# Kernel tuning notes

Hardware: AMD Instinct MI355X
Metric: run time of the kernel (lower is better)

The kernel has to match this reference:

```python
import math
import jax, jax.numpy as jnp
import numpy as np

D = 1024
H = 16
DK = D // H
B = 4
L = 2048


def setup_inputs() -> dict:
    key = jax.random.key(0)
    ks = jax.random.split(key, 11)
    s = 1.0 / math.sqrt(D)
    return {
        "q": jax.random.normal(ks[0], (B, L, D), jnp.float32),
        "k": jax.random.normal(ks[1], (B, L, D), jnp.float32),
        "v": jax.random.normal(ks[2], (B, L, D), jnp.float32),
        "wq_w": jax.random.normal(ks[3], (D, D), jnp.float32) * s,
        "wq_b": jnp.zeros((D,), jnp.float32),
        "wk_w": jax.random.normal(ks[4], (D, D), jnp.float32) * s,
        "wk_b": jnp.zeros((D,), jnp.float32),
        "wv_w": jax.random.normal(ks[5], (D, D), jnp.float32) * s,
        "wv_b": jnp.zeros((D,), jnp.float32),
        "wo_w": jax.random.normal(ks[6], (D, D), jnp.float32) * s,
        "wo_b": jnp.zeros((D,), jnp.float32),
    }


def reference(q, k, v, wq_w, wq_b, wk_w, wk_b, wv_w, wv_b, wo_w, wo_b):
    # torch Linear: x @ W.T + b
    Q = (q @ wq_w.T + wq_b).reshape(B, L, H, DK).transpose(0, 2, 1, 3)  # [B,H,L,DK]
    K = (k @ wk_w.T + wk_b).reshape(B, -1, H, DK).transpose(0, 2, 1, 3)
    V = (v @ wv_w.T + wv_b).reshape(B, -1, H, DK).transpose(0, 2, 1, 3)
    sc = jnp.einsum("bhqd,bhkd->bhqk", Q, K) / math.sqrt(DK)  # [B,H,L,L]
    # causal mask: strictly upper triangular filled with -1e9
    cm = jnp.triu(jnp.ones((L, L), dtype=bool), 1)
    sc = jnp.where(cm, jnp.float32(-1e9), sc)
    at = jax.nn.softmax(sc, axis=-1)  # dropout p=0 (eval)
    out = jnp.einsum("bhqk,bhkd->bhqd", at, V)  # [B,H,L,DK]
    out = out.transpose(0, 2, 1, 3).reshape(B, L, D)
    return out @ wo_w.T + wo_b
```

## Files before the change

kernel.cpp:

```cpp
#include <hip/hip_runtime.h>
#include <stdint.h>

#define DD 1024
#define NH 16
#define DHEAD 64
#define NB 4
#define SEQ 2048
#define MR (NB*SEQ)
#define NT (SEQ/128)

typedef __attribute__((ext_vector_type(8))) short s8v;
typedef __attribute__((ext_vector_type(4))) float f4v;

__device__ __forceinline__ unsigned short f2bf(float f) {
  union { float f; uint32_t u; } c; c.f = f;
  uint32_t u = c.u;
  u += 0x7fffu + ((u >> 16) & 1u);
  return (unsigned short)(u >> 16);
}
__device__ __forceinline__ unsigned short f2bf_trunc(float f) {
  union { float f; uint32_t u; } c; c.f = f;
  return (unsigned short)(c.u >> 16);
}

__device__ __forceinline__ void load_lds16(const void* g, void* lds) {
  __builtin_amdgcn_global_load_lds(
      (__attribute__((address_space(1))) void*)(uintptr_t)g,
      (__attribute__((address_space(3))) void*)(uint32_t)(uintptr_t)lds,
      16, 0, 0);
}

__device__ __forceinline__ s8v pack8(float4 a, float4 b) {
  union { unsigned short us[8]; s8v v; } t;
  t.us[0] = f2bf(a.x); t.us[1] = f2bf(a.y); t.us[2] = f2bf(a.z); t.us[3] = f2bf(a.w);
  t.us[4] = f2bf(b.x); t.us[5] = f2bf(b.y); t.us[6] = f2bf(b.z); t.us[7] = f2bf(b.w);
  return t.v;
}

__global__ void cvt_w(
    const float* __restrict__ w0, const float* __restrict__ w1,
    const float* __restrict__ w2, const float* __restrict__ w3,
    unsigned short* __restrict__ d0, unsigned short* __restrict__ d1,
    unsigned short* __restrict__ d2, unsigned short* __restrict__ d3)
{
  int blk = blockIdx.x;
  int a = blk >> 9;
  const float* src = a == 0 ? w0 : (a == 1 ? w1 : (a == 2 ? w2 : w3));
  unsigned short* dst = a == 0 ? d0 : (a == 1 ? d1 : (a == 2 ? d2 : d3));
  size_t i = (size_t)(blk & 511) * 2048 + (size_t)threadIdx.x * 8;
  float4 a4 = *(const float4*)(src + i);
  float4 b4 = *(const float4*)(src + i + 4);
  union { unsigned short us[8]; uint4 u; } t;
  t.us[0] = f2bf(a4.x); t.us[1] = f2bf(a4.y); t.us[2] = f2bf(a4.z); t.us[3] = f2bf(a4.w);
  t.us[4] = f2bf(b4.x); t.us[5] = f2bf(b4.y); t.us[6] = f2bf(b4.z); t.us[7] = f2bf(b4.w);
  *(uint4*)(dst + i) = t.u;
}

__global__ __launch_bounds__(256, 2) void gemm_bt(
    const unsigned short* __restrict__ A,
    const unsigned short* __restrict__ Bw,
    const float* __restrict__ bias,
    float* __restrict__ Cout)
{
  __shared__ __align__(16) short As[64 * 64];
  __shared__ __align__(16) short Bs[128 * 64];
  const int linear = blockIdx.y * 8 + blockIdx.x;
  const int nx = linear >> 7;
  const int my = linear & 127;
  const int tid = threadIdx.x;
  const int wave = tid >> 6, lane = tid & 63;
  const int wm = (wave >> 1) * 32, wn = (wave & 1) * 64;
  const int lr = lane & 15, lg = lane >> 4;
  const int sw = lr & 7;
  const unsigned short* Ab = A + (size_t)my * 64 * DD;
  const unsigned short* Bb = Bw + (size_t)nx * 128 * DD;

  f4v z = {0.f, 0.f, 0.f, 0.f};
  f4v acc[2][4];
  for (int mi = 0; mi < 2; mi++) for (int ni = 0; ni < 4; ni++) acc[mi][ni] = z;

  for (int k0 = 0; k0 < DD; k0 += 64) {
    __syncthreads();
    for (int i = 0; i < 2; i++) {
      int c = tid + i * 256;
      int row = c >> 3, pg = c & 7;
      load_lds16(Ab + (size_t)row * DD + k0 + ((pg ^ (row & 7)) << 3), As + c * 8);
    }
    for (int i = 0; i < 4; i++) {
      int c = tid + i * 256;
      int row = c >> 3, pg = c & 7;
      load_lds16(Bb + (size_t)row * DD + k0 + ((pg ^ (row & 7)) << 3), Bs + c * 8);
    }
    __syncthreads();
    for (int kk = 0; kk < 64; kk += 32) {
      int gb = kk >> 3;
      s8v af[2], bf[4];
      for (int i = 0; i < 2; i++)
        af[i] = *(const s8v*)(As + (wm + i * 16 + lr) * 64 + (((gb + lg) ^ sw) << 3));
      for (int i = 0; i < 4; i++)
        bf[i] = *(const s8v*)(Bs + (wn + i * 16 + lr) * 64 + (((gb + lg) ^ sw) << 3));
      for (int mi = 0; mi < 2; mi++)
        for (int ni = 0; ni < 4; ni++)
          acc[mi][ni] = __builtin_amdgcn_mfma_f32_16x16x32_bf16(af[mi], bf[ni], acc[mi][ni], 0, 0, 0);
    }
  }
  for (int ni = 0; ni < 4; ni++) {
    int col = nx * 128 + wn + ni * 16 + lr;
    float bv = bias[col];
    for (int mi = 0; mi < 2; mi++) {
      int row0 = my * 64 + wm + mi * 16 + lg * 4;
      for (int r = 0; r < 4; r++)
        Cout[(size_t)(row0 + r) * DD + col] = acc[mi][ni][r] + bv;
    }
  }
}

__global__ __launch_bounds__(256, 2) void gemm_qkv(
    const float* __restrict__ qA, const float* __restrict__ kA,
    const float* __restrict__ vA,
    const unsigned short* __restrict__ wq, const unsigned short* __restrict__ wk,
    const unsigned short* __restrict__ wv,
    const float* __restrict__ bq, const float* __restrict__ bk, const float* __restrict__ bv,
    unsigned short* __restrict__ Qp, unsigned short* __restrict__ Kp,
    unsigned short* __restrict__ VpT)
{
  __shared__ __align__(16) short As[128 * 64];
  __shared__ __align__(16) short Bs[128 * 64];
  const int linear = blockIdx.y * 24 + blockIdx.x;
  const int nx  = linear / 192;
  const int rem = linear % 192;
  const int seg = rem >> 6;
  const int my  = rem & 63;
  const float* A          = seg == 0 ? qA : (seg == 1 ? kA : vA);
  const unsigned short* Bw = seg == 0 ? wq : (seg == 1 ? wk : wv);
  const float* bias        = seg == 0 ? bq : (seg == 1 ? bk : bv);

  const int tid = threadIdx.x;
  const int wave = tid >> 6, lane = tid & 63;
  const int wm = (wave >> 1) * 64, wn = (wave & 1) * 64;
  const int lr = lane & 15, lg = lane >> 4;
  const int sw = lr & 7;
  const float* Ab = A + (size_t)my * 128 * DD;
  const unsigned short* Bb = Bw + (size_t)nx * 128 * DD;

  int arow[4], ag[4];
  s8v areg[4];
  for (int i = 0; i < 4; i++) {
    int c = tid + i * 256;
    arow[i] = c >> 3; ag[i] = c & 7;
  }
  for (int i = 0; i < 4; i++) {
    const float* src = Ab + (size_t)arow[i] * DD + (ag[i] << 3);
    areg[i] = pack8(*(const float4*)src, *(const float4*)(src + 4));
  }

  f4v z = {0.f, 0.f, 0.f, 0.f};
  f4v acc[4][4];
  for (int mi = 0; mi < 4; mi++) for (int ni = 0; ni < 4; ni++) acc[mi][ni] = z;

  for (int k0 = 0; k0 < DD; k0 += 64) {
    __syncthreads();
    for (int i = 0; i < 4; i++)
      *(s8v*)(As + arow[i] * 64 + ((ag[i] ^ (arow[i] & 7)) << 3)) = areg[i];
    for (int i = 0; i < 4; i++) {
      int c = tid + i * 256;
      int row = c >> 3, pg = c & 7;
      load_lds16(Bb + (size_t)row * DD + k0 + ((pg ^ (row & 7)) << 3), Bs + c * 8);
    }
    __syncthreads();
    if (k0 + 64 < DD) {
      for (int i = 0; i < 4; i++) {
        const float* src = Ab + (size_t)arow[i] * DD + k0 + 64 + (ag[i] << 3);
        areg[i] = pack8(*(const float4*)src, *(const float4*)(src + 4));
      }
    }
    for (int kk = 0; kk < 64; kk += 32) {
      int gb = kk >> 3;
      s8v af[4], bf[4];
      for (int i = 0; i < 4; i++)
        af[i] = *(const s8v*)(As + (wm + i * 16 + lr) * 64 + (((gb + lg) ^ sw) << 3));
      for (int i = 0; i < 4; i++)
        bf[i] = *(const s8v*)(Bs + (wn + i * 16 + lr) * 64 + (((gb + lg) ^ sw) << 3));
      for (int mi = 0; mi < 4; mi++)
        for (int ni = 0; ni < 4; ni++)
          acc[mi][ni] = __builtin_amdgcn_mfma_f32_16x16x32_bf16(af[mi], bf[ni], acc[mi][ni], 0, 0, 0);
    }
  }
  if (seg < 2) {
    unsigned short* Cout = seg == 0 ? Qp : Kp;
    for (int ni = 0; ni < 4; ni++) {
      int col = nx * 128 + wn + ni * 16 + lr;
      float bv = bias[col];
      for (int mi = 0; mi < 4; mi++) {
        int row0 = my * 128 + wm + mi * 16 + lg * 4;
        for (int r = 0; r < 4; r++)
          Cout[(size_t)(row0 + r) * DD + col] = f2bf(acc[mi][ni][r] + bv);
      }
    }
  } else {
    for (int ni = 0; ni < 4; ni++) {
      int col = nx * 128 + wn + ni * 16 + lr;
      float bv = bias[col];
      int hh = col >> 6, dd = col & 63;
      for (int mi = 0; mi < 4; mi++) {
        int row0 = my * 128 + wm + mi * 16 + lg * 4;
        int bb = row0 >> 11, ll = row0 & 2047;
        uint64_t w = 0;
        for (int r = 0; r < 4; r++)
          w |= (uint64_t)f2bf(acc[mi][ni][r] + bv) << (16 * r);
        *(uint64_t*)(VpT + ((size_t)(bb * NH + hh) * 64 + dd) * SEQ + ll) = w;
      }
    }
  }
}

#define KS_STRIDE 72
#define VT_STRIDE 136
#define PS_STRIDE 72

__device__ __forceinline__ void attn_step(
    const s8v (&qf)[2][2], const s8v (&kf)[2][4],
    f4v (&o)[2][4], float (&ls)[2][4],
    int qbase, int colbase,
    const short* __restrict__ Vt, int vsub, short* __restrict__ Pw,
    int lr, int lg)
{
  const float csc = 0.125f * 1.44269504089f;
  const float FM = 14.0f;
  f4v zv = {0.f, 0.f, 0.f, 0.f};
  f4v s[2][4];
  for (int mi = 0; mi < 2; mi++) for (int ni = 0; ni < 4; ni++) s[mi][ni] = zv;
  for (int ks = 0; ks < 2; ks++)
    for (int mi = 0; mi < 2; mi++)
      for (int ni = 0; ni < 4; ni++)
        s[mi][ni] = __builtin_amdgcn_mfma_f32_16x16x32_bf16(qf[mi][ks], kf[ks][ni], s[mi][ni], 0, 0, 0);
  const bool diag = (colbase + 63 > qbase);
  for (int mi = 0; mi < 2; mi++)
    for (int ni = 0; ni < 4; ni++)
      for (int r = 0; r < 4; r++) {
        float e = __builtin_amdgcn_exp2f(fmaf(s[mi][ni][r], csc, -FM));
        if (diag) {
          int row = qbase + mi * 16 + lg * 4 + r;
          int col = colbase + ni * 16 + lr;
          e = (col > row) ? 0.f : e;
        }
        ls[mi][r] += e;
        Pw[(mi * 16 + lg * 4 + r) * PS_STRIDE + ni * 16 + lr] = (short)f2bf_trunc(e);
      }
  for (int kc2 = 0; kc2 < 2; kc2++) {
    s8v pf[2], vf[4];
    for (int mi = 0; mi < 2; mi++)
      pf[mi] = *(const s8v*)(Pw + (mi * 16 + lr) * PS_STRIDE + kc2 * 32 + lg * 8);
    for (int ni = 0; ni < 4; ni++)
      vf[ni] = *(const s8v*)(Vt + (ni * 16 + lr) * VT_STRIDE + vsub + kc2 * 32 + lg * 8);
    for (int mi = 0; mi < 2; mi++)
      for (int ni = 0; ni < 4; ni++)
        o[mi][ni] = __builtin_amdgcn_mfma_f32_16x16x32_bf16(pf[mi], vf[ni], o[mi][ni], 0, 0, 0);
  }
}

__global__ __launch_bounds__(256, 2) void fattn(
    const unsigned short* __restrict__ Qp,
    const unsigned short* __restrict__ Kp,
    const unsigned short* __restrict__ VpT,
    unsigned short* __restrict__ Op)
{
  __shared__ __align__(16) short Ks[128 * KS_STRIDE];
  __shared__ __align__(16) short Vt[64 * VT_STRIDE];
  __shared__ __align__(16) short Ps[4 * 32 * PS_STRIDE];
  const int tid = threadIdx.x;
  const int wave = tid >> 6, lane = tid & 63;
  const int lr = lane & 15, lg = lane >> 4;
  const int linear = blockIdx.y * 8 + blockIdx.x;
  const int xA = linear >> 6;
  const int bh = linear & 63;
  const int b = bh >> 4, h = bh & 15;
  const int xB = NT - 1 - xA;
  const int qbA = xA * 128 + wave * 32;
  const int qbB = xB * 128 + wave * 32;
  const unsigned short* Qrow = Qp + ((size_t)b * SEQ) * DD + h * DHEAD;
  const unsigned short* Krow = Kp + ((size_t)b * SEQ) * DD + h * DHEAD;
  const unsigned short* VT   = VpT + (size_t)bh * 64 * SEQ;
  short* Pw = Ps + wave * (32 * PS_STRIDE);

  s8v qfA[2][2], qfB[2][2];
  for (int mi = 0; mi < 2; mi++)
    for (int ks = 0; ks < 2; ks++) {
      qfA[mi][ks] = *(const s8v*)(Qrow + (size_t)(qbA + mi * 16 + lr) * DD + ks * 32 + lg * 8);
      qfB[mi][ks] = *(const s8v*)(Qrow + (size_t)(qbB + mi * 16 + lr) * DD + ks * 32 + lg * 8);
    }

  f4v zv = {0.f, 0.f, 0.f, 0.f};
  f4v oA[2][4], oB[2][4];
  float lA[2][4], lB[2][4];
  for (int mi = 0; mi < 2; mi++)
    for (int r = 0; r < 4; r++) { lA[mi][r] = 0.f; lB[mi][r] = 0.f; }
  for (int mi = 0; mi < 2; mi++)
    for (int ni = 0; ni < 4; ni++) { oA[mi][ni] = zv; oB[mi][ni] = zv; }

  const int npair = xB + 1;

  for (int p = 0; p < npair; p++) {
    s8v kreg[4], vreg[4];
    int krow[4], kkc[4], vd[4], vkc[4];
    for (int i = 0; i < 4; i++) {
      int c = tid + i * 256;
      krow[i] = c >> 3; kkc[i] = (c & 7) << 3;
      kreg[i] = *(const s8v*)(Krow + (size_t)(p * 128 + krow[i]) * DD + kkc[i]);
      vd[i] = c >> 4; vkc[i] = (c & 15) << 3;
      vreg[i] = *(const s8v*)(VT + (size_t)vd[i] * SEQ + p * 128 + vkc[i]);
    }
    __syncthreads();
    for (int i = 0; i < 4; i++) {
      *(s8v*)(Ks + krow[i] * KS_STRIDE + kkc[i]) = kreg[i];
      *(s8v*)(Vt + vd[i] * VT_STRIDE + vkc[i]) = vreg[i];
    }
    __syncthreads();
    for (int sub = 0; sub < 2; sub++) {
      int colbase = (2 * p + sub) * 64;
      bool actB = colbase <= qbB + 31;
      bool actA = colbase <= qbA + 31;
      if (actB || actA) {
        const short* KsSub = Ks + sub * 64 * KS_STRIDE;
        s8v kf[2][4];
        for (int ks = 0; ks < 2; ks++)
          for (int ni = 0; ni < 4; ni++)
            kf[ks][ni] = *(const s8v*)(KsSub + (ni * 16 + lr) * KS_STRIDE + ks * 32 + lg * 8);
        int vsub = sub * 64;
        if (actB) attn_step(qfB, kf, oB, lB, qbB, colbase, Vt, vsub, Pw, lr, lg);
        if (actA) attn_step(qfA, kf, oA, lA, qbA, colbase, Vt, vsub, Pw, lr, lg);
      }
    }
  }

  unsigned short* Orow = Op + ((size_t)b * SEQ) * DD + h * DHEAD;
  for (int mi = 0; mi < 2; mi++)
    for (int r = 0; r < 4; r++) {
      float sA = lA[mi][r], sB = lB[mi][r];
      for (int d2 = 1; d2 < 16; d2 <<= 1) {
        sA += __shfl_xor(sA, d2);
        sB += __shfl_xor(sB, d2);
      }
      float invA = 1.f / sA, invB = 1.f / sB;
      size_t rowA = (size_t)qbA + mi * 16 + lg * 4 + r;
      size_t rowB = (size_t)qbB + mi * 16 + lg * 4 + r;
      for (int ni = 0; ni < 4; ni++) {
        Orow[rowA * DD + ni * 16 + lr] = f2bf(oA[mi][ni][r] * invA);
        Orow[rowB * DD + ni * 16 + lr] = f2bf(oB[mi][ni][r] * invB);
      }
    }
}

extern "C" void kernel_launch(void* const* d_in, const int* in_sizes, int n_in,
                              void* d_out, int out_size, void* d_ws, size_t ws_size,
                              hipStream_t stream) {
  const float* q    = (const float*)d_in[0];
  const float* k    = (const float*)d_in[1];
  const float* v    = (const float*)d_in[2];
  const float* wq_w = (const float*)d_in[3];
  const float* wq_b = (const float*)d_in[4];
  const float* wk_w = (const float*)d_in[5];
  const float* wk_b = (const float*)d_in[6];
  const float* wv_w = (const float*)d_in[7];
  const float* wv_b = (const float*)d_in[8];
  const float* wo_w = (const float*)d_in[9];
  const float* wo_b = (const float*)d_in[10];

  const size_t BIG = (size_t)MR * DD;
  const size_t WSZ = (size_t)DD * DD;
  unsigned short* p = (unsigned short*)d_ws;
  unsigned short* wqb = p; p += WSZ;
  unsigned short* wkb = p; p += WSZ;
  unsigned short* wvb = p; p += WSZ;
  unsigned short* wob = p; p += WSZ;
  unsigned short* Qp  = p; p += BIG;
  unsigned short* Kp  = p; p += BIG;
  unsigned short* VpT = p; p += BIG;
  unsigned short* AO  = p; p += BIG;

  cvt_w<<<dim3(2048), dim3(256), 0, stream>>>(
      wq_w, wk_w, wv_w, wo_w, wqb, wkb, wvb, wob);

  gemm_qkv<<<dim3(24, MR / 128), dim3(256), 0, stream>>>(
      q, k, v, wqb, wkb, wvb, wq_b, wk_b, wv_b, Qp, Kp, VpT);

  fattn<<<dim3(NT / 2, NB * NH), dim3(256), 0, stream>>>(Qp, Kp, VpT, AO);

  gemm_bt<<<dim3(8, 128), dim3(256), 0, stream>>>(AO, wob, wo_b, (float*)d_out);

  (void)in_sizes; (void)n_in; (void)out_size; (void)ws_size;
}
```

Measured before the change: 313.1 us.

## Pre-convert QKV activations to bf16 and enlarge output GEMM tile

Adds a separate kernel that converts the q, k and v activations to bf16 in scratch buffers, reusing the AO workspace and the output buffer as scratch. The QKV GEMM can then stage A through direct global-to-LDS loads instead of register loads with in-loop packing. The output projection GEMM moves from 64x128 to 128x128 tiles to get more reuse per block. The cost is an extra full pass that reads and writes the activations, and half as many blocks for the output GEMM.

```diff
diff --git a/kernel.cpp b/kernel.cpp
--- a/kernel.cpp
+++ b/kernel.cpp
@@ -28,13 +28,6 @@
       (__attribute__((address_space(1))) void*)(uintptr_t)g,
       (__attribute__((address_space(3))) void*)(uint32_t)(uintptr_t)lds,
       16, 0, 0);
-}
-
-__device__ __forceinline__ s8v pack8(float4 a, float4 b) {
-  union { unsigned short us[8]; s8v v; } t;
-  t.us[0] = f2bf(a.x); t.us[1] = f2bf(a.y); t.us[2] = f2bf(a.z); t.us[3] = f2bf(a.w);
-  t.us[4] = f2bf(b.x); t.us[5] = f2bf(b.y); t.us[6] = f2bf(b.z); t.us[7] = f2bf(b.w);
-  return t.v;
 }
 
 __global__ void cvt_w(
@@ -56,32 +49,51 @@
   *(uint4*)(dst + i) = t.u;
 }
 
+__global__ void cvt_a(
+    const float* __restrict__ s0, const float* __restrict__ s1,
+    const float* __restrict__ s2,
+    unsigned short* __restrict__ d0, unsigned short* __restrict__ d1,
+    unsigned short* __restrict__ d2)
+{
+  int blk = blockIdx.x;
+  int a = blk >> 12;
+  const float* src = a == 0 ? s0 : (a == 1 ? s1 : s2);
+  unsigned short* dst = a == 0 ? d0 : (a == 1 ? d1 : d2);
+  size_t i = (size_t)(blk & 4095) * 2048 + (size_t)threadIdx.x * 8;
+  float4 a4 = *(const float4*)(src + i);
+  float4 b4 = *(const float4*)(src + i + 4);
+  union { unsigned short us[8]; uint4 u; } t;
+  t.us[0] = f2bf(a4.x); t.us[1] = f2bf(a4.y); t.us[2] = f2bf(a4.z); t.us[3] = f2bf(a4.w);
+  t.us[4] = f2bf(b4.x); t.us[5] = f2bf(b4.y); t.us[6] = f2bf(b4.z); t.us[7] = f2bf(b4.w);
+  *(uint4*)(dst + i) = t.u;
+}
+
 __global__ __launch_bounds__(256, 2) void gemm_bt(
     const unsigned short* __restrict__ A,
     const unsigned short* __restrict__ Bw,
     const float* __restrict__ bias,
     float* __restrict__ Cout)
 {
-  __shared__ __align__(16) short As[64 * 64];
+  __shared__ __align__(16) short As[128 * 64];
   __shared__ __align__(16) short Bs[128 * 64];
   const int linear = blockIdx.y * 8 + blockIdx.x;
-  const int nx = linear >> 7;
-  const int my = linear & 127;
+  const int nx = linear >> 6;
+  const int my = linear & 63;
   const int tid = threadIdx.x;
   const int wave = tid >> 6, lane = tid & 63;
-  const int wm = (wave >> 1) * 32, wn = (wave & 1) * 64;
+  const int wm = (wave >> 1) * 64, wn = (wave & 1) * 64;
   const int lr = lane & 15, lg = lane >> 4;
   const int sw = lr & 7;
-  const unsigned short* Ab = A + (size_t)my * 64 * DD;
+  const unsigned short* Ab = A + (size_t)my * 128 * DD;
   const unsigned short* Bb = Bw + (size_t)nx * 128 * DD;
 
   f4v z = {0.f, 0.f, 0.f, 0.f};
-  f4v acc[2][4];
-  for (int mi = 0; mi < 2; mi++) for (int ni = 0; ni < 4; ni++) acc[mi][ni] = z;
+  f4v acc[4][4];
+  for (int mi = 0; mi < 4; mi++) for (int ni = 0; ni < 4; ni++) acc[mi][ni] = z;
 
   for (int k0 = 0; k0 < DD; k0 += 64) {
     __syncthreads();
-    for (int i = 0; i < 2; i++) {
+    for (int i = 0; i < 4; i++) {
       int c = tid + i * 256;
       int row = c >> 3, pg = c & 7;
       load_lds16(Ab + (size_t)row * DD + k0 + ((pg ^ (row & 7)) << 3), As + c * 8);
@@ -94,12 +106,12 @@
     __syncthreads();
     for (int kk = 0; kk < 64; kk += 32) {
       int gb = kk >> 3;
-      s8v af[2], bf[4];
-      for (int i = 0; i < 2; i++)
+      s8v af[4], bf[4];
+      for (int i = 0; i < 4; i++)
         af[i] = *(const s8v*)(As + (wm + i * 16 + lr) * 64 + (((gb + lg) ^ sw) << 3));
       for (int i = 0; i < 4; i++)
         bf[i] = *(const s8v*)(Bs + (wn + i * 16 + lr) * 64 + (((gb + lg) ^ sw) << 3));
-      for (int mi = 0; mi < 2; mi++)
+      for (int mi = 0; mi < 4; mi++)
         for (int ni = 0; ni < 4; ni++)
           acc[mi][ni] = __builtin_amdgcn_mfma_f32_16x16x32_bf16(af[mi], bf[ni], acc[mi][ni], 0, 0, 0);
     }
@@ -107,8 +119,8 @@
   for (int ni = 0; ni < 4; ni++) {
     int col = nx * 128 + wn + ni * 16 + lr;
     float bv = bias[col];
-    for (int mi = 0; mi < 2; mi++) {
-      int row0 = my * 64 + wm + mi * 16 + lg * 4;
+    for (int mi = 0; mi < 4; mi++) {
+      int row0 = my * 128 + wm + mi * 16 + lg * 4;
       for (int r = 0; r < 4; r++)
         Cout[(size_t)(row0 + r) * DD + col] = acc[mi][ni][r] + bv;
     }
@@ -116,8 +128,8 @@
 }
 
 __global__ __launch_bounds__(256, 2) void gemm_qkv(
-    const float* __restrict__ qA, const float* __restrict__ kA,
-    const float* __restrict__ vA,
+    const unsigned short* __restrict__ qA, const unsigned short* __restrict__ kA,
+    const unsigned short* __restrict__ vA,
     const unsigned short* __restrict__ wq, const unsigned short* __restrict__ wk,
     const unsigned short* __restrict__ wv,
     const float* __restrict__ bq, const float* __restrict__ bk, const float* __restrict__ bv,
@@ -131,7 +143,7 @@
   const int rem = linear % 192;
   const int seg = rem >> 6;
   const int my  = rem & 63;
-  const float* A          = seg == 0 ? qA : (seg == 1 ? kA : vA);
+  const unsigned short* A  = seg == 0 ? qA : (seg == 1 ? kA : vA);
   const unsigned short* Bw = seg == 0 ? wq : (seg == 1 ? wk : wv);
   const float* bias        = seg == 0 ? bq : (seg == 1 ? bk : bv);
 
@@ -140,19 +152,8 @@
   const int wm = (wave >> 1) * 64, wn = (wave & 1) * 64;
   const int lr = lane & 15, lg = lane >> 4;
   const int sw = lr & 7;
-  const float* Ab = A + (size_t)my * 128 * DD;
+  const unsigned short* Ab = A + (size_t)my * 128 * DD;
   const unsigned short* Bb = Bw + (size_t)nx * 128 * DD;
-
-  int arow[4], ag[4];
-  s8v areg[4];
-  for (int i = 0; i < 4; i++) {
-    int c = tid + i * 256;
-    arow[i] = c >> 3; ag[i] = c & 7;
-  }
-  for (int i = 0; i < 4; i++) {
-    const float* src = Ab + (size_t)arow[i] * DD + (ag[i] << 3);
-    areg[i] = pack8(*(const float4*)src, *(const float4*)(src + 4));
-  }
 
   f4v z = {0.f, 0.f, 0.f, 0.f};
   f4v acc[4][4];
@@ -160,20 +161,17 @@
 
   for (int k0 = 0; k0 < DD; k0 += 64) {
     __syncthreads();
-    for (int i = 0; i < 4; i++)
-      *(s8v*)(As + arow[i] * 64 + ((ag[i] ^ (arow[i] & 7)) << 3)) = areg[i];
+    for (int i = 0; i < 4; i++) {
+      int c = tid + i * 256;
+      int row = c >> 3, pg = c & 7;
+      load_lds16(Ab + (size_t)row * DD + k0 + ((pg ^ (row & 7)) << 3), As + c * 8);
+    }
     for (int i = 0; i < 4; i++) {
       int c = tid + i * 256;
       int row = c >> 3, pg = c & 7;
       load_lds16(Bb + (size_t)row * DD + k0 + ((pg ^ (row & 7)) << 3), Bs + c * 8);
     }
     __syncthreads();
-    if (k0 + 64 < DD) {
-      for (int i = 0; i < 4; i++) {
-        const float* src = Ab + (size_t)arow[i] * DD + k0 + 64 + (ag[i] << 3);
-        areg[i] = pack8(*(const float4*)src, *(const float4*)(src + 4));
-      }
-    }
     for (int kk = 0; kk < 64; kk += 32) {
       int gb = kk >> 3;
       s8v af[4], bf[4];
@@ -378,15 +376,21 @@
   unsigned short* VpT = p; p += BIG;
   unsigned short* AO  = p; p += BIG;
 
+  unsigned short* qb = AO;
+  unsigned short* kb = (unsigned short*)d_out;
+  unsigned short* vb = kb + BIG;
+
   cvt_w<<<dim3(2048), dim3(256), 0, stream>>>(
       wq_w, wk_w, wv_w, wo_w, wqb, wkb, wvb, wob);
 
+  cvt_a<<<dim3(12288), dim3(256), 0, stream>>>(q, k, v, qb, kb, vb);
+
   gemm_qkv<<<dim3(24, MR / 128), dim3(256), 0, stream>>>(
-      q, k, v, wqb, wkb, wvb, wq_b, wk_b, wv_b, Qp, Kp, VpT);
+      qb, kb, vb, wqb, wkb, wvb, wq_b, wk_b, wv_b, Qp, Kp, VpT);
 
   fattn<<<dim3(NT / 2, NB * NH), dim3(256), 0, stream>>>(Qp, Kp, VpT, AO);
 
-  gemm_bt<<<dim3(8, 128), dim3(256), 0, stream>>>(AO, wob, wo_b, (float*)d_out);
+  gemm_bt<<<dim3(8, MR / 128), dim3(256), 0, stream>>>(AO, wob, wo_b, (float*)d_out);
 
   (void)in_sizes; (void)n_in; (void)out_size; (void)ws_size;
 }
```

Result: no change. 314.0 us (+0.3%).
